# Performance work log

Hardware: AMD Instinct MI355X
Metric: run time of the kernel (lower is better)

The kernel has to match this reference:

```python
import jax, jax.numpy as jnp
import numpy as np

B, N, NODE, EDIM, LAT, ENC = 4, 512, 3, 1, 32, 32
NEG = -jnp.inf


def _xavier(key, fan_in, fan_out):
    a = jnp.sqrt(6.0 / (fan_in + fan_out))
    return jax.random.uniform(key, (fan_in, fan_out), jnp.float32, -a, a)


def _mpnn(z, enc_e, adj_b, Wm, Wu):
    """Message: linear([z_i, z_j, e_ij]); adjacency-masked max-aggregation; update linear."""
    zd = z.shape[-1]
    zi = jnp.broadcast_to(z[:, :, None, :], (B, N, N, zd))
    zj = jnp.broadcast_to(z[:, None, :, :], (B, N, N, zd))
    msg = jnp.concatenate([zi, zj, enc_e], axis=-1) @ Wm          # [B,N,N,LAT]
    msg = jnp.where(adj_b[..., None], msg, NEG)
    agg = jnp.max(msg, axis=2)                                    # max over neighbors j
    return jnp.concatenate([z, agg], axis=-1) @ Wu                # [B,N,LAT]


def setup_inputs() -> dict:
    key = jax.random.key(0)
    ks = jax.random.split(key, 16)
    x = jax.random.normal(ks[0], (B, N, NODE), jnp.float32)
    h = jax.random.normal(ks[1], (B, N, LAT), jnp.float32)
    adj = jax.random.randint(ks[2], (B, N, N), 0, 2, jnp.int32)
    e_feat = jax.random.uniform(ks[3], (B, N, N, EDIM), jnp.float32)
    Wn = _xavier(ks[4], LAT + NODE, ENC)          # node_encoder
    We = _xavier(ks[5], EDIM, ENC)                # edge_encoder
    Wm = _xavier(ks[6], 2 * ENC + ENC, LAT)       # processor message
    Wu = _xavier(ks[7], ENC + LAT, LAT)           # processor update
    Wtm = _xavier(ks[8], 2 * LAT + ENC, LAT)      # termination_mpnn message
    Wtu = _xavier(ks[9], LAT + LAT, LAT)          # termination_mpnn update
    Wd = _xavier(ks[10], LAT + ENC, NODE)         # decoder
    Wt = _xavier(ks[11], LAT, 1)                  # termination head
    Wp = _xavier(ks[12], 2 * LAT + ENC, 1)        # predecessor head (pred=1)
    return {"x": x, "h": h, "adj": adj, "e_feat": e_feat, "Wn": Wn, "We": We,
            "Wm": Wm, "Wu": Wu, "Wtm": Wtm, "Wtu": Wtu, "Wd": Wd, "Wt": Wt, "Wp": Wp}


def reference(x, h, adj, e_feat, Wn, We, Wm, Wu, Wtm, Wtu, Wd, Wt, Wp):
    adj2 = adj + jnp.eye(N, dtype=adj.dtype)[None]                # add self-loops
    adj_b = adj2.astype(bool)
    z = jnp.concatenate([x, h], axis=-1) @ Wn                     # [B,N,ENC]
    enc_e = e_feat @ We                                           # [B,N,N,ENC]
    new_h = _mpnn(z, enc_e, adj_b, Wm, Wu) + z                    # [B,N,LAT]
    new_x = jnp.concatenate([z, new_h], axis=-1) @ Wd             # [B,N,NODE]
    tau_node = _mpnn(new_h, enc_e, adj_b, Wtm, Wtu)               # [B,N,LAT]
    tau = jnp.mean(tau_node, axis=1) @ Wt                         # [B,1]
    # predecessor head: all-pairs [h_i, h_j, e_ij] -> scalar, masked by adjacency
    hi = jnp.broadcast_to(new_h[:, :, None, :], (B, N, N, LAT))
    hj = jnp.broadcast_to(new_h[:, None, :, :], (B, N, N, LAT))
    p = (jnp.concatenate([hi, hj, enc_e], axis=-1) @ Wp)[..., 0]  # [B,N,N]
    p = jnp.where(adj_b, p, NEG)
    return new_x, p, tau, new_h
```

## Files before the change

kernel.cpp:

```cpp
#include <hip/hip_runtime.h>

#define XN 512
#define XB 4
#define XNEG  (-3.402823466e38f)
#define XMASK (-1.0e38f)

__device__ __forceinline__ float xscrub(float v) {
    unsigned u = __float_as_uint(v);
    u = ((u & 0x7f800000u) == 0x7f800000u) ? 0xff7fffffu : u;
    return __uint_as_float(u);
}

__global__ __launch_bounds__(64) void ne2v_g0(
    const float* __restrict__ We, const float* __restrict__ Wm,
    const float* __restrict__ Wtm, const float* __restrict__ Wtu,
    const float* __restrict__ Wt, const float* __restrict__ Wp,
    float* __restrict__ drv, float* __restrict__ tau_out)
{
    const int t = threadIdx.x;
    if (t < 32) {
        float c1 = 0.f, c2 = 0.f;
        for (int k = 0; k < 32; ++k) {
            const float w = We[k];
            c1 += w * Wm[(64 + k) * 32 + t];
            c2 += w * Wtm[(64 + k) * 32 + t];
        }
        drv[t]      = c1;
        drv[32 + t] = c2;
        float u1 = 0.f, u2 = 0.f;
        for (int k = 0; k < 32; ++k) {
            u1 += Wtu[t * 32 + k]        * Wt[k];
            u2 += Wtu[(32 + t) * 32 + k] * Wt[k];
        }
        drv[64 + t] = u1;
        drv[96 + t] = u2;
        if (t == 0) {
            float cp = 0.f;
            for (int k = 0; k < 32; ++k) cp += We[k] * Wp[64 + k];
            drv[128] = cp;
        }
    }
    if (t < XB) tau_out[t] = 0.f;
}

__global__ __launch_bounds__(256) void ne2v_g1(
    const float* __restrict__ x, const float* __restrict__ h,
    const float* __restrict__ Wn, const float* __restrict__ Wm,
    float* __restrict__ z, float* __restrict__ A1, float* __restrict__ B1)
{
    const int t = threadIdx.x;
    const int r = t >> 5;
    const int l = t & 31;
    const int row = blockIdx.x * 8 + r;
    float acc = 0.f;
    {
        const float* xr = x + row * 3;
        const float* hr = h + row * 32;
        for (int k = 0; k < 3; ++k)  acc += xr[k] * Wn[k * 32 + l];
        for (int k = 0; k < 32; ++k) acc += hr[k] * Wn[(3 + k) * 32 + l];
    }
    __shared__ float zs[8][32];
    zs[r][l] = acc;
    z[row * 32 + l] = acc;
    __syncthreads();
    float a = 0.f, bb = 0.f;
    for (int k = 0; k < 32; ++k) {
        const float zk = zs[r][k];
        a  += zk * Wm[k * 32 + l];
        bb += zk * Wm[(32 + k) * 32 + l];
    }
    A1[row * 32 + l] = a;
    B1[row * 32 + l] = bb;
}

__global__ __launch_bounds__(256) void ne2v_m2(
    const int* __restrict__ adj, const float* __restrict__ ef,
    const float* __restrict__ z, const float* __restrict__ A1,
    const float* __restrict__ B1, const float* __restrict__ drv,
    const float* __restrict__ Wu, const float* __restrict__ Wd,
    const float* __restrict__ Wtm, const float* __restrict__ Wp,
    float* __restrict__ A2, float* __restrict__ B2,
    float* __restrict__ hp1, float* __restrict__ hp2,
    float* __restrict__ o_newx, float* __restrict__ o_newh)
{
    const int q = blockIdx.x;
    const int b = q >> 8;
    const int i0 = (q & 255) * 2;
    const int row0 = b * XN + i0;
    const int t = threadIdx.x;

    __shared__ float emf[2 * XN];
    __shared__ float adf[2 * XN];
    __shared__ float wush[64 * 32];
    __shared__ float wtmsh[64 * 32];
    __shared__ float wdsh[192];
    __shared__ float wpsh[64];
    __shared__ float zsf[64], a1sf[64], ags[64], nhs[64];
    __shared__ float red[2][8][33];

    const float c1v = drv[t & 31];
    {
        const int*   ab = adj + (size_t)row0 * XN;
        const float* eb = ef  + (size_t)row0 * XN;
        for (int u = t; u < 2 * XN; u += 256) {
            const int r = u >> 9, j = u & (XN - 1);
            const int on = (ab[u] != 0) | (j == i0 + r);
            emf[j * 2 + r] = on ? eb[u] : 0.f;
            adf[j * 2 + r] = on ? 0.f : XMASK;
        }
        const float4* wu4 = (const float4*)Wu;
        const float4* wt4 = (const float4*)Wtm;
        ((float4*)wush)[t]        = wu4[t];
        ((float4*)wush)[t + 256]  = wu4[t + 256];
        ((float4*)wtmsh)[t]       = wt4[t];
        ((float4*)wtmsh)[t + 256] = wt4[t + 256];
        if (t < 192) wdsh[t] = Wd[t];
        if (t < 64)  wpsh[t] = Wp[t];
        if (t < 64) { zsf[t] = z[row0 * 32 + t]; a1sf[t] = A1[row0 * 32 + t]; }
    }
    __syncthreads();

    const int c = t >> 5, l = t & 31;
    const float* Bp = B1 + (size_t)b * XN * 32 + l;
    const int j0 = c * 64;
    float m0 = XNEG, m1 = XNEG;
#pragma unroll 16
    for (int k = 0; k < 64; ++k) {
        const int j = j0 + k;
        const float bv = Bp[(size_t)j * 32];
        m0 = fmaxf(m0, fmaf(emf[j * 2],     c1v, bv) + adf[j * 2]);
        m1 = fmaxf(m1, fmaf(emf[j * 2 + 1], c1v, bv) + adf[j * 2 + 1]);
    }
    red[0][c][l] = m0;
    red[1][c][l] = m1;
    __syncthreads();

    if (t < 64) {
        const int r = t >> 5, ll = t & 31;
        float mm = red[r][0][ll];
        for (int cc = 1; cc < 8; ++cc) mm = fmaxf(mm, red[r][cc][ll]);
        ags[t] = a1sf[t] + mm;
    }
    __syncthreads();

    if (t < 64) {
        const int r = t >> 5, ll = t & 31;
        float v = zsf[t];
        for (int k = 0; k < 32; ++k)
            v += zsf[r * 32 + k] * wush[k * 32 + ll]
               + ags[r * 32 + k] * wush[(32 + k) * 32 + ll];
        nhs[t] = v;
        o_newh[row0 * 32 + t] = v;
    }
    __syncthreads();

    if (t < 64) {
        const int r = t >> 5, ll = t & 31;
        float a2 = 0.f, b2 = 0.f;
        for (int k = 0; k < 32; ++k) {
            const float nk = nhs[r * 32 + k];
            a2 += nk * wtmsh[k * 32 + ll];
            b2 += nk * wtmsh[(32 + k) * 32 + ll];
        }
        A2[row0 * 32 + t] = a2;
        B2[row0 * 32 + t] = b2;
    } else if (t >= 128 && t < 132) {
        const int r = (t - 128) >> 1, which = (t - 128) & 1;
        float p = 0.f;
        for (int k = 0; k < 32; ++k) p += nhs[r * 32 + k] * wpsh[which * 32 + k];
        (which ? hp2 : hp1)[row0 + r] = p;
    } else if (t >= 160 && t < 166) {
        const int idx = t - 160, r = idx / 3, d = idx % 3;
        float v = 0.f;
        for (int k = 0; k < 32; ++k)
            v += zsf[r * 32 + k] * wdsh[k * 3 + d]
               + nhs[r * 32 + k] * wdsh[(32 + k) * 3 + d];
        o_newx[(row0 + r) * 3 + d] = v;
    }
}

__global__ __launch_bounds__(256) void ne2v_m3(
    const int* __restrict__ adj, const float* __restrict__ ef,
    const float* __restrict__ A2, const float* __restrict__ B2,
    const float* __restrict__ newh, const float* __restrict__ hp1,
    const float* __restrict__ hp2, const float* __restrict__ drv,
    float* __restrict__ o_p, float* __restrict__ tau_out)
{
    const int q = blockIdx.x;
    const int b = q >> 8;
    const int i0 = (q & 255) * 2;
    const int row0 = b * XN + i0;
    const int t = threadIdx.x;

    __shared__ float emf[2 * XN];
    __shared__ float adf[2 * XN];
    __shared__ float hp2s[XN];
    __shared__ float a2sf[64], nhsf[64], ss[64];
    __shared__ float red[2][8][33];

    const float c2v = drv[32 + (t & 31)];
    const float cpv = drv[128];
    const float h1a = hp1[row0];
    const float h1b = hp1[row0 + 1];
    {
        const int*   ab = adj + (size_t)row0 * XN;
        const float* eb = ef  + (size_t)row0 * XN;
        for (int u = t; u < 2 * XN; u += 256) {
            const int r = u >> 9, j = u & (XN - 1);
            const int on = (ab[u] != 0) | (j == i0 + r);
            emf[j * 2 + r] = on ? eb[u] : 0.f;
            adf[j * 2 + r] = on ? 0.f : XMASK;
        }
        for (int u = t; u < XN; u += 256) hp2s[u] = hp2[b * XN + u];
        if (t < 64) { a2sf[t] = A2[row0 * 32 + t]; nhsf[t] = newh[row0 * 32 + t]; }
    }
    __syncthreads();

    {
        float* pr0 = o_p + (size_t)row0 * XN;
        float* pr1 = pr0 + XN;
        for (int j = t; j < XN; j += 256) {
            pr0[j] = xscrub(h1a + hp2s[j] + emf[j * 2]     * cpv + adf[j * 2]);
            pr1[j] = xscrub(h1b + hp2s[j] + emf[j * 2 + 1] * cpv + adf[j * 2 + 1]);
        }
    }

    const int c = t >> 5, l = t & 31;
    const float* Bp = B2 + (size_t)b * XN * 32 + l;
    const int j0 = c * 64;
    float m0 = XNEG, m1 = XNEG;
#pragma unroll 16
    for (int k = 0; k < 64; ++k) {
        const int j = j0 + k;
        const float bv = Bp[(size_t)j * 32];
        m0 = fmaxf(m0, fmaf(emf[j * 2],     c2v, bv) + adf[j * 2]);
        m1 = fmaxf(m1, fmaf(emf[j * 2 + 1], c2v, bv) + adf[j * 2 + 1]);
    }
    red[0][c][l] = m0;
    red[1][c][l] = m1;
    __syncthreads();

    if (t < 64) {
        const int r = t >> 5, ll = t & 31;
        float mm = red[r][0][ll];
        for (int cc = 1; cc < 8; ++cc) mm = fmaxf(mm, red[r][cc][ll]);
        const float agg = a2sf[t] + mm;
        ss[t] = nhsf[t] * drv[64 + ll] + agg * drv[96 + ll];
    }
    __syncthreads();
    if (t < 64) {
        float s = ss[t];
        s += __shfl_down(s, 32);
        s += __shfl_down(s, 16);
        s += __shfl_down(s, 8);
        s += __shfl_down(s, 4);
        s += __shfl_down(s, 2);
        s += __shfl_down(s, 1);
        if (t == 0) atomicAdd(&tau_out[b], s * (1.0f / XN));
    }
}

extern "C" void kernel_launch(void* const* d_in, const int* in_sizes, int n_in,
                              void* d_out, int out_size, void* d_ws, size_t ws_size,
                              hipStream_t stream)
{
    const float* x   = (const float*)d_in[0];
    const float* h   = (const float*)d_in[1];
    const int*   adj = (const int*)  d_in[2];
    const float* ef  = (const float*)d_in[3];
    const float* Wn  = (const float*)d_in[4];
    const float* We  = (const float*)d_in[5];
    const float* Wm  = (const float*)d_in[6];
    const float* Wu  = (const float*)d_in[7];
    const float* Wtm = (const float*)d_in[8];
    const float* Wtu = (const float*)d_in[9];
    const float* Wd  = (const float*)d_in[10];
    const float* Wt  = (const float*)d_in[11];
    const float* Wp  = (const float*)d_in[12];

    float* out    = (float*)d_out;
    float* o_newx = out;
    float* o_p    = out + 6144;
    float* o_tau  = out + 6144 + XB * XN * XN;
    float* o_newh = o_tau + XB;

    float* w = (float*)d_ws;
    const int RN = XB * XN * 32;
    float* z   = w;
    float* A1  = w + RN;
    float* B1  = w + 2 * RN;
    float* A2  = w + 3 * RN;
    float* B2  = w + 4 * RN;
    float* hp1 = w + 5 * RN;
    float* hp2 = w + 5 * RN + XB * XN;
    float* drv = w + 5 * RN + 2 * XB * XN;

    hipLaunchKernelGGL(ne2v_g0, dim3(1), dim3(64), 0, stream,
                       We, Wm, Wtm, Wtu, Wt, Wp, drv, o_tau);
    hipLaunchKernelGGL(ne2v_g1, dim3(XB * XN / 8), dim3(256), 0, stream,
                       x, h, Wn, Wm, z, A1, B1);
    hipLaunchKernelGGL(ne2v_m2, dim3(XB * XN / 2), dim3(256), 0, stream,
                       adj, ef, z, A1, B1, drv, Wu, Wd, Wtm, Wp,
                       A2, B2, hp1, hp2, o_newx, o_newh);
    hipLaunchKernelGGL(ne2v_m3, dim3(XB * XN / 2), dim3(256), 0, stream,
                       adj, ef, A2, B2, o_newh, hp1, hp2, drv, o_p, o_tau);
}
```

Measured before the change: 118.5 us.

## Fuse all stages into one persistent kernel with software grid barriers

Replaces the four-kernel pipeline with a small init kernel plus one 1024-block kernel that computes node encodings, the two MPNN layers and the predecessor head, separated by atomic-counter grid barriers. Adjacency and edge features are loaded into shared memory once and reused by both message-passing phases instead of being reloaded, and per-row intermediates stay in shared memory. This removes launch overhead and global round-trips of z/A1/A2. The cost is that every block must be co-resident (256 threads, launch_bounds min 4 blocks per CU); if they are not, the spin-wait deadlocks or hits its bounded timeout. The small derived weight products are now recomputed in every block.

```diff
diff --git a/kernel.cpp b/kernel.cpp
--- a/kernel.cpp
+++ b/kernel.cpp
@@ -4,6 +4,7 @@
 #define XB 4
 #define XNEG  (-3.402823466e38f)
 #define XMASK (-1.0e38f)
+#define NBLK 1024
 
 __device__ __forceinline__ float xscrub(float v) {
     unsigned u = __float_as_uint(v);
@@ -11,77 +12,48 @@
     return __uint_as_float(u);
 }
 
-__global__ __launch_bounds__(64) void ne2v_g0(
-    const float* __restrict__ We, const float* __restrict__ Wm,
+__global__ __launch_bounds__(64) void ne2p_init(unsigned* __restrict__ bar,
+                                                float* __restrict__ tau)
+{
+    if (threadIdx.x < 2) bar[threadIdx.x] = 0u;
+    if (threadIdx.x < XB) tau[threadIdx.x] = 0.f;
+}
+
+__device__ __forceinline__ void gridbar(unsigned* __restrict__ cnt,
+                                        unsigned* __restrict__ gen)
+{
+    __syncthreads();
+    if (threadIdx.x == 0) {
+        __threadfence();
+        const unsigned g = __hip_atomic_load(gen, __ATOMIC_RELAXED, __HIP_MEMORY_SCOPE_AGENT);
+        const unsigned a = __hip_atomic_fetch_add(cnt, 1u, __ATOMIC_ACQ_REL, __HIP_MEMORY_SCOPE_AGENT) + 1u;
+        if (a == (unsigned)NBLK) {
+            __hip_atomic_store(cnt, 0u, __ATOMIC_RELAXED, __HIP_MEMORY_SCOPE_AGENT);
+            __hip_atomic_fetch_add(gen, 1u, __ATOMIC_RELEASE, __HIP_MEMORY_SCOPE_AGENT);
+        } else {
+            long it = 0;
+            while (__hip_atomic_load(gen, __ATOMIC_ACQUIRE, __HIP_MEMORY_SCOPE_AGENT) == g) {
+                __builtin_amdgcn_s_sleep(2);
+                if (++it > (1L << 27)) break;
+            }
+        }
+        __threadfence();
+    }
+    __syncthreads();
+}
+
+__global__ __launch_bounds__(256, 4) void ne2p_all(
+    const float* __restrict__ x, const float* __restrict__ h,
+    const int* __restrict__ adj, const float* __restrict__ ef,
+    const float* __restrict__ Wn, const float* __restrict__ We,
+    const float* __restrict__ Wm, const float* __restrict__ Wu,
     const float* __restrict__ Wtm, const float* __restrict__ Wtu,
-    const float* __restrict__ Wt, const float* __restrict__ Wp,
-    float* __restrict__ drv, float* __restrict__ tau_out)
-{
-    const int t = threadIdx.x;
-    if (t < 32) {
-        float c1 = 0.f, c2 = 0.f;
-        for (int k = 0; k < 32; ++k) {
-            const float w = We[k];
-            c1 += w * Wm[(64 + k) * 32 + t];
-            c2 += w * Wtm[(64 + k) * 32 + t];
-        }
-        drv[t]      = c1;
-        drv[32 + t] = c2;
-        float u1 = 0.f, u2 = 0.f;
-        for (int k = 0; k < 32; ++k) {
-            u1 += Wtu[t * 32 + k]        * Wt[k];
-            u2 += Wtu[(32 + t) * 32 + k] * Wt[k];
-        }
-        drv[64 + t] = u1;
-        drv[96 + t] = u2;
-        if (t == 0) {
-            float cp = 0.f;
-            for (int k = 0; k < 32; ++k) cp += We[k] * Wp[64 + k];
-            drv[128] = cp;
-        }
-    }
-    if (t < XB) tau_out[t] = 0.f;
-}
-
-__global__ __launch_bounds__(256) void ne2v_g1(
-    const float* __restrict__ x, const float* __restrict__ h,
-    const float* __restrict__ Wn, const float* __restrict__ Wm,
-    float* __restrict__ z, float* __restrict__ A1, float* __restrict__ B1)
-{
-    const int t = threadIdx.x;
-    const int r = t >> 5;
-    const int l = t & 31;
-    const int row = blockIdx.x * 8 + r;
-    float acc = 0.f;
-    {
-        const float* xr = x + row * 3;
-        const float* hr = h + row * 32;
-        for (int k = 0; k < 3; ++k)  acc += xr[k] * Wn[k * 32 + l];
-        for (int k = 0; k < 32; ++k) acc += hr[k] * Wn[(3 + k) * 32 + l];
-    }
-    __shared__ float zs[8][32];
-    zs[r][l] = acc;
-    z[row * 32 + l] = acc;
-    __syncthreads();
-    float a = 0.f, bb = 0.f;
-    for (int k = 0; k < 32; ++k) {
-        const float zk = zs[r][k];
-        a  += zk * Wm[k * 32 + l];
-        bb += zk * Wm[(32 + k) * 32 + l];
-    }
-    A1[row * 32 + l] = a;
-    B1[row * 32 + l] = bb;
-}
-
-__global__ __launch_bounds__(256) void ne2v_m2(
-    const int* __restrict__ adj, const float* __restrict__ ef,
-    const float* __restrict__ z, const float* __restrict__ A1,
-    const float* __restrict__ B1, const float* __restrict__ drv,
-    const float* __restrict__ Wu, const float* __restrict__ Wd,
-    const float* __restrict__ Wtm, const float* __restrict__ Wp,
-    float* __restrict__ A2, float* __restrict__ B2,
-    float* __restrict__ hp1, float* __restrict__ hp2,
-    float* __restrict__ o_newx, float* __restrict__ o_newh)
+    const float* __restrict__ Wd, const float* __restrict__ Wt,
+    const float* __restrict__ Wp,
+    float* __restrict__ B1g, float* __restrict__ B2g, float* __restrict__ hp2g,
+    unsigned* __restrict__ bar,
+    float* __restrict__ o_newx, float* __restrict__ o_p,
+    float* __restrict__ o_tau, float* __restrict__ o_newh)
 {
     const int q = blockIdx.x;
     const int b = q >> 8;
@@ -91,14 +63,14 @@
 
     __shared__ float emf[2 * XN];
     __shared__ float adf[2 * XN];
-    __shared__ float wush[64 * 32];
-    __shared__ float wtmsh[64 * 32];
-    __shared__ float wdsh[192];
-    __shared__ float wpsh[64];
-    __shared__ float zsf[64], a1sf[64], ags[64], nhs[64];
+    __shared__ float wush[2048], wtmsh[2048];
+    __shared__ float wdsh[192], wpsh[64];
+    __shared__ float drvs[132];
+    __shared__ float zs[64], a1s[64], ags[64], nhs[64], a2s[64], ssx[64];
     __shared__ float red[2][8][33];
-
-    const float c1v = drv[t & 31];
+    __shared__ float hp2s[XN];
+    __shared__ float hp1s[2];
+
     {
         const int*   ab = adj + (size_t)row0 * XN;
         const float* eb = ef  + (size_t)row0 * XN;
@@ -116,44 +88,87 @@
         ((float4*)wtmsh)[t + 256] = wt4[t + 256];
         if (t < 192) wdsh[t] = Wd[t];
         if (t < 64)  wpsh[t] = Wp[t];
-        if (t < 64) { zsf[t] = z[row0 * 32 + t]; a1sf[t] = A1[row0 * 32 + t]; }
-    }
-    __syncthreads();
+    }
+    if (t < 64) {
+        const int r = t >> 5, l = t & 31;
+        const int row = row0 + r;
+        const float* xr = x + row * 3;
+        const float* hr = h + row * 32;
+        float acc = 0.f;
+        for (int k = 0; k < 3; ++k)  acc += xr[k] * Wn[k * 32 + l];
+        for (int k = 0; k < 32; ++k) acc += hr[k] * Wn[(3 + k) * 32 + l];
+        zs[t] = acc;
+    } else if (t < 96) {
+        const int l = t - 64;
+        float c1 = 0.f, c2 = 0.f;
+        for (int k = 0; k < 32; ++k) {
+            const float w = We[k];
+            c1 += w * Wm[(64 + k) * 32 + l];
+            c2 += w * Wtm[(64 + k) * 32 + l];
+        }
+        drvs[l] = c1; drvs[32 + l] = c2;
+    } else if (t < 128) {
+        const int l = t - 96;
+        float u1 = 0.f, u2 = 0.f;
+        for (int k = 0; k < 32; ++k) {
+            u1 += Wtu[l * 32 + k]        * Wt[k];
+            u2 += Wtu[(32 + l) * 32 + k] * Wt[k];
+        }
+        drvs[64 + l] = u1; drvs[96 + l] = u2;
+    } else if (t == 128) {
+        float cp = 0.f;
+        for (int k = 0; k < 32; ++k) cp += We[k] * Wp[64 + k];
+        drvs[128] = cp;
+    }
+    __syncthreads();
+    if (t < 64) {
+        const int r = t >> 5, l = t & 31;
+        float a = 0.f, bb = 0.f;
+        for (int k = 0; k < 32; ++k) {
+            const float zk = zs[r * 32 + k];
+            a  += zk * Wm[k * 32 + l];
+            bb += zk * Wm[(32 + k) * 32 + l];
+        }
+        a1s[t] = a;
+        B1g[row0 * 32 + t] = bb;
+    }
+
+    gridbar(bar, bar + 1);
 
     const int c = t >> 5, l = t & 31;
-    const float* Bp = B1 + (size_t)b * XN * 32 + l;
-    const int j0 = c * 64;
-    float m0 = XNEG, m1 = XNEG;
-#pragma unroll 16
-    for (int k = 0; k < 64; ++k) {
-        const int j = j0 + k;
-        const float bv = Bp[(size_t)j * 32];
-        m0 = fmaxf(m0, fmaf(emf[j * 2],     c1v, bv) + adf[j * 2]);
-        m1 = fmaxf(m1, fmaf(emf[j * 2 + 1], c1v, bv) + adf[j * 2 + 1]);
-    }
-    red[0][c][l] = m0;
-    red[1][c][l] = m1;
-    __syncthreads();
-
+    {
+        const float c1v = drvs[l];
+        const float* Bp = B1g + (size_t)b * XN * 32 + l;
+        const int j0 = c * 64;
+        float m0 = XNEG, m1 = XNEG;
+#pragma unroll 8
+        for (int k = 0; k < 64; ++k) {
+            const int j = j0 + k;
+            const float bv = Bp[(size_t)j * 32];
+            m0 = fmaxf(m0, fmaf(emf[j * 2],     c1v, bv) + adf[j * 2]);
+            m1 = fmaxf(m1, fmaf(emf[j * 2 + 1], c1v, bv) + adf[j * 2 + 1]);
+        }
+        red[0][c][l] = m0;
+        red[1][c][l] = m1;
+    }
+    __syncthreads();
     if (t < 64) {
         const int r = t >> 5, ll = t & 31;
         float mm = red[r][0][ll];
         for (int cc = 1; cc < 8; ++cc) mm = fmaxf(mm, red[r][cc][ll]);
-        ags[t] = a1sf[t] + mm;
-    }
-    __syncthreads();
-
-    if (t < 64) {
-        const int r = t >> 5, ll = t & 31;
-        float v = zsf[t];
+        ags[t] = a1s[t] + mm;
+    }
+    __syncthreads();
+    if (t < 64) {
+        const int r = t >> 5, ll = t & 31;
+        float v = zs[t];
         for (int k = 0; k < 32; ++k)
-            v += zsf[r * 32 + k] * wush[k * 32 + ll]
+            v += zs[r * 32 + k] * wush[k * 32 + ll]
                + ags[r * 32 + k] * wush[(32 + k) * 32 + ll];
         nhs[t] = v;
         o_newh[row0 * 32 + t] = v;
     }
     __syncthreads();
-
     if (t < 64) {
         const int r = t >> 5, ll = t & 31;
         float a2 = 0.f, b2 = 0.f;
@@ -162,61 +177,29 @@
             a2 += nk * wtmsh[k * 32 + ll];
             b2 += nk * wtmsh[(32 + k) * 32 + ll];
         }
-        A2[row0 * 32 + t] = a2;
-        B2[row0 * 32 + t] = b2;
+        a2s[t] = a2;
+        B2g[row0 * 32 + t] = b2;
     } else if (t >= 128 && t < 132) {
         const int r = (t - 128) >> 1, which = (t - 128) & 1;
         float p = 0.f;
         for (int k = 0; k < 32; ++k) p += nhs[r * 32 + k] * wpsh[which * 32 + k];
-        (which ? hp2 : hp1)[row0 + r] = p;
+        if (which) hp2g[b * XN + i0 + r] = p; else hp1s[r] = p;
     } else if (t >= 160 && t < 166) {
         const int idx = t - 160, r = idx / 3, d = idx % 3;
         float v = 0.f;
         for (int k = 0; k < 32; ++k)
-            v += zsf[r * 32 + k] * wdsh[k * 3 + d]
+            v += zs[r * 32 + k] * wdsh[k * 3 + d]
                + nhs[r * 32 + k] * wdsh[(32 + k) * 3 + d];
         o_newx[(row0 + r) * 3 + d] = v;
     }
-}
-
-__global__ __launch_bounds__(256) void ne2v_m3(
-    const int* __restrict__ adj, const float* __restrict__ ef,
-    const float* __restrict__ A2, const float* __restrict__ B2,
-    const float* __restrict__ newh, const float* __restrict__ hp1,
-    const float* __restrict__ hp2, const float* __restrict__ drv,
-    float* __restrict__ o_p, float* __restrict__ tau_out)
-{
-    const int q = blockIdx.x;
-    const int b = q >> 8;
-    const int i0 = (q & 255) * 2;
-    const int row0 = b * XN + i0;
-    const int t = threadIdx.x;
-
-    __shared__ float emf[2 * XN];
-    __shared__ float adf[2 * XN];
-    __shared__ float hp2s[XN];
-    __shared__ float a2sf[64], nhsf[64], ss[64];
-    __shared__ float red[2][8][33];
-
-    const float c2v = drv[32 + (t & 31)];
-    const float cpv = drv[128];
-    const float h1a = hp1[row0];
-    const float h1b = hp1[row0 + 1];
-    {
-        const int*   ab = adj + (size_t)row0 * XN;
-        const float* eb = ef  + (size_t)row0 * XN;
-        for (int u = t; u < 2 * XN; u += 256) {
-            const int r = u >> 9, j = u & (XN - 1);
-            const int on = (ab[u] != 0) | (j == i0 + r);
-            emf[j * 2 + r] = on ? eb[u] : 0.f;
-            adf[j * 2 + r] = on ? 0.f : XMASK;
-        }
-        for (int u = t; u < XN; u += 256) hp2s[u] = hp2[b * XN + u];
-        if (t < 64) { a2sf[t] = A2[row0 * 32 + t]; nhsf[t] = newh[row0 * 32 + t]; }
-    }
-    __syncthreads();
-
-    {
+
+    gridbar(bar, bar + 1);
+
+    for (int u = t; u < XN; u += 256) hp2s[u] = hp2g[b * XN + u];
+    __syncthreads();
+    {
+        const float cpv = drvs[128];
+        const float h1a = hp1s[0], h1b = hp1s[1];
         float* pr0 = o_p + (size_t)row0 * XN;
         float* pr1 = pr0 + XN;
         for (int j = t; j < XN; j += 256) {
@@ -224,39 +207,39 @@
             pr1[j] = xscrub(h1b + hp2s[j] + emf[j * 2 + 1] * cpv + adf[j * 2 + 1]);
         }
     }
-
-    const int c = t >> 5, l = t & 31;
-    const float* Bp = B2 + (size_t)b * XN * 32 + l;
-    const int j0 = c * 64;
-    float m0 = XNEG, m1 = XNEG;
-#pragma unroll 16
-    for (int k = 0; k < 64; ++k) {
-        const int j = j0 + k;
-        const float bv = Bp[(size_t)j * 32];
-        m0 = fmaxf(m0, fmaf(emf[j * 2],     c2v, bv) + adf[j * 2]);
-        m1 = fmaxf(m1, fmaf(emf[j * 2 + 1], c2v, bv) + adf[j * 2 + 1]);
-    }
-    red[0][c][l] = m0;
-    red[1][c][l] = m1;
-    __syncthreads();
-
+    {
+        const float c2v = drvs[32 + l];
+        const float* Bp = B2g + (size_t)b * XN * 32 + l;
+        const int j0 = c * 64;
+        float m0 = XNEG, m1 = XNEG;
+#pragma unroll 8
+        for (int k = 0; k < 64; ++k) {
+            const int j = j0 + k;
+            const float bv = Bp[(size_t)j * 32];
+            m0 = fmaxf(m0, fmaf(emf[j * 2],     c2v, bv) + adf[j * 2]);
+            m1 = fmaxf(m1, fmaf(emf[j * 2 + 1], c2v, bv) + adf[j * 2 + 1]);
+        }
+        red[0][c][l] = m0;
+        red[1][c][l] = m1;
+    }
+    __syncthreads();
     if (t < 64) {
         const int r = t >> 5, ll = t & 31;
         float mm = red[r][0][ll];
         for (int cc = 1; cc < 8; ++cc) mm = fmaxf(mm, red[r][cc][ll]);
-        const float agg = a2sf[t] + mm;
-        ss[t] = nhsf[t] * drv[64 + ll] + agg * drv[96 + ll];
-    }
-    __syncthreads();
-    if (t < 64) {
-        float s = ss[t];
+        const float agg = a2s[t] + mm;
+        ssx[t] = nhs[t] * drvs[64 + ll] + agg * drvs[96 + ll];
+    }
+    __syncthreads();
+    if (t < 64) {
+        float s = ssx[t];
         s += __shfl_down(s, 32);
         s += __shfl_down(s, 16);
         s += __shfl_down(s, 8);
         s += __shfl_down(s, 4);
         s += __shfl_down(s, 2);
         s += __shfl_down(s, 1);
-        if (t == 0) atomicAdd(&tau_out[b], s * (1.0f / XN));
+        if (t == 0) atomicAdd(&o_tau[b], s * (1.0f / XN));
     }
 }
 
@@ -286,22 +269,13 @@
 
     float* w = (float*)d_ws;
     const int RN = XB * XN * 32;
-    float* z   = w;
-    float* A1  = w + RN;
-    float* B1  = w + 2 * RN;
-    float* A2  = w + 3 * RN;
-    float* B2  = w + 4 * RN;
-    float* hp1 = w + 5 * RN;
-    float* hp2 = w + 5 * RN + XB * XN;
-    float* drv = w + 5 * RN + 2 * XB * XN;
-
-    hipLaunchKernelGGL(ne2v_g0, dim3(1), dim3(64), 0, stream,
-                       We, Wm, Wtm, Wtu, Wt, Wp, drv, o_tau);
-    hipLaunchKernelGGL(ne2v_g1, dim3(XB * XN / 8), dim3(256), 0, stream,
-                       x, h, Wn, Wm, z, A1, B1);
-    hipLaunchKernelGGL(ne2v_m2, dim3(XB * XN / 2), dim3(256), 0, stream,
-                       adj, ef, z, A1, B1, drv, Wu, Wd, Wtm, Wp,
-                       A2, B2, hp1, hp2, o_newx, o_newh);
-    hipLaunchKernelGGL(ne2v_m3, dim3(XB * XN / 2), dim3(256), 0, stream,
-                       adj, ef, A2, B2, o_newh, hp1, hp2, drv, o_p, o_tau);
-}
+    float*    B1g  = w;
+    float*    B2g  = w + RN;
+    float*    hp2g = w + 2 * RN;
+    unsigned* bar  = (unsigned*)(w + 2 * RN + XB * XN);
+
+    hipLaunchKernelGGL(ne2p_init, dim3(1), dim3(64), 0, stream, bar, o_tau);
+    hipLaunchKernelGGL(ne2p_all, dim3(NBLK), dim3(256), 0, stream,
+                       x, h, adj, ef, Wn, We, Wm, Wu, Wtm, Wtu, Wd, Wt, Wp,
+                       B1g, B2g, hp2g, bar, o_newx, o_p, o_tau, o_newh);
+}
```

Result: slower. 334.2 us (+182.0%).
